# Kernel optimization log

Hardware: AMD Instinct MI355X
Metric: run time of the kernel (lower is better)

Reference implementation:

```python
import jax, jax.numpy as jnp
import numpy as np
from jax.scipy.special import gammaln, digamma


def setup_inputs() -> dict:
    key = jax.random.key(0)
    k1, k2 = jax.random.split(key)
    N, M, D = 512, 512, 256
    # Dirichlet concentration parameters: strictly positive
    v_alpha = jax.random.uniform(k1, (N, D), dtype=jnp.float32)
    t_alpha = jax.random.uniform(k2, (M, D), dtype=jnp.float32)
    return {"v_alpha": v_alpha, "t_alpha": t_alpha}


def _compute_kl(v_alpha, t_alpha):
    # v_alpha, t_alpha broadcast to (..., D); returns (...,) KL(Dir(v)||Dir(t))
    eps = 1e-08
    v = v_alpha + eps
    t = t_alpha + eps
    sum_v = v.sum(axis=-1)
    sum_t = t.sum(axis=-1)
    first = (gammaln(t).sum(axis=-1) + gammaln(sum_v)
             - gammaln(sum_t) - gammaln(v).sum(axis=-1))
    second = ((v - t) * (digamma(v) - digamma(sum_v)[..., None])).sum(axis=-1)
    return first + second


def reference(v_alpha, t_alpha):
    # Pairwise JS divergence between all (t_row, v_row) pairs.
    # Original: v.repeat(M,1) / t.repeat_interleave(N) then view(M, N)
    # -> equivalent to broadcasting t over axis 0, v over axis 1.
    v = v_alpha[None, :, :]   # (1, N, D)
    t = t_alpha[:, None, :]   # (M, 1, D)
    m = 0.5 * (v + t)         # (M, N, D)
    jsd = 0.5 * _compute_kl(v, m) + 0.5 * _compute_kl(t, m)  # (M, N)
    return 1.0 - jsd
```

## Files before the change

### kernel.cpp

```cpp
#include <hip/hip_runtime.h>

#define D 256
#define NV 512
#define NT 512
#define EPS 1e-8f
#define HALF_EPS 5e-9f
#define LN2 0.69314718055994531f

#define C0 0.28468287047291920f
#define C1 0.70315664064524320f
#define C2 0.24517887805011740f
#define C3 (-0.03936734194028790f)
#define C4 0.00932941036738560f
#define C5 (-0.00261463332905590f)
#define C6 0.00080356830356760f
#define C0E 0.28460998445f
#define C1E 0.69577526404f
#define C2E 0.24751123064f

#define LSTRIDE 68

__device__ __forceinline__ float rcpf(float x) { return __builtin_amdgcn_rcpf(x); }

__device__ __forceinline__ float stirling_lgamma(float y) {
    float r = rcpf(y), r2 = r * r;
    float ln = LN2 * __log2f(y);
    return (y - 0.5f) * ln - y + 0.91893853320467f
         + r * (0.08333333333f - 0.00277777778f * r2);
}

__device__ __forceinline__ float stirling_digamma(float y) {
    float r = rcpf(y), r2 = r * r;
    return LN2 * __log2f(y) - 0.5f * r - r2 * (0.08333333333f - 0.00833333333f * r2);
}

__global__ __launch_bounds__(256) void row_stats(
    const float* __restrict__ va, const float* __restrict__ ta,
    float* __restrict__ dgv, float* __restrict__ dgt,
    float* __restrict__ rv,  float* __restrict__ rt)
{
    int r = blockIdx.x;
    const float* row; float* dgrow; float* sc;
    if (r < NV) { row = va + r * D; dgrow = dgv + r * D; sc = rv + r * 4; }
    else { int q = r - NV; row = ta + q * D; dgrow = dgt + q * D; sc = rt + q * 4; }

    int d = threadIdx.x;
    float raw = row[d];
    float x = raw + EPS;

    float y = x + 4.0f;
    float ry = rcpf(y), ry2 = ry * ry;
    float psi = LN2 * __log2f(y) - 0.5f * ry - ry2 * (0.08333333333f - 0.00833333333f * ry2);
    psi -= rcpf(x) + rcpf(x + 1.0f) + rcpf(x + 2.0f) + rcpf(x + 3.0f);
    dgrow[d] = psi;

    float s = x - 0.5f;
    float q6 = fmaf(C6, s, C5);
    q6 = fmaf(q6, s, C4); q6 = fmaf(q6, s, C3); q6 = fmaf(q6, s, C2); q6 = fmaf(q6, s, C1);
    float g = fmaf(q6, s, C0) - LN2 * __log2f(x * (x + 1.0f));

    float S = raw, G = g, P = raw * psi, W = psi;
    #pragma unroll
    for (int off = 32; off > 0; off >>= 1) {
        S += __shfl_down(S, off, 64);
        G += __shfl_down(G, off, 64);
        P += __shfl_down(P, off, 64);
        W += __shfl_down(W, off, 64);
    }
    __shared__ float red[4][4];
    int wid = d >> 6, lane = d & 63;
    if (lane == 0) { red[0][wid] = S; red[1][wid] = G; red[2][wid] = P; red[3][wid] = W; }
    __syncthreads();
    if (d == 0) {
        float S4 = red[0][0] + red[0][1] + red[0][2] + red[0][3];
        float G4 = red[1][0] + red[1][1] + red[1][2] + red[1][3];
        float P4 = red[2][0] + red[2][1] + red[2][2] + red[2][3];
        float W4 = red[3][0] + red[3][1] + red[3][2] + red[3][3];
        float Se = S4 + 256.0f * EPS;
        float A = 0.5f * (stirling_lgamma(Se) - G4) + 0.25f * P4 + (0.25f * EPS) * W4;
        *(float4*)sc = make_float4(S4, A, stirling_digamma(Se), 0.0f);
    }
}

__global__ __launch_bounds__(256, 4) void jsd_pairs(
    const float* __restrict__ va, const float* __restrict__ ta,
    const float* __restrict__ dgv, const float* __restrict__ dgt,
    const float* __restrict__ rv,  const float* __restrict__ rt,
    float* __restrict__ out)
{
    __shared__ float vs[16 * LSTRIDE];
    __shared__ float gv[16 * LSTRIDE];
    __shared__ float ts[16 * LSTRIDE];
    __shared__ float gt[16 * LSTRIDE];

    const int tid = threadIdx.x;
    const int j0 = blockIdx.x * 16;
    const int i0 = blockIdx.y * 16;

    const int tj = tid & 15;
    const int ti = tid >> 4;

    const float* vp = vs + tj * LSTRIDE;
    const float* gp = gv + tj * LSTRIDE;
    const float* tp = ts + ti * LSTRIDE;
    const float* hp = gt + ti * LSTRIDE;
    const int ldst = ti * LSTRIDE + (tj << 2);

    float accM2a = 0.0f, accM2b = 0.0f;
    float accLa = 0.0f, accLb = 0.0f;
    float xsa = 0.0f, xsb = 0.0f;

    for (int h = 0; h < 4; ++h) {
        if (h) __syncthreads();
        {
            int goff = (h << 6) + (tj << 2);
            float4 a = *(const float4*)(va  + (j0 + ti) * D + goff);
            float4 b = *(const float4*)(dgv + (j0 + ti) * D + goff);
            float4 e = *(const float4*)(ta  + (i0 + ti) * D + goff);
            float4 f = *(const float4*)(dgt + (i0 + ti) * D + goff);
            a.x = fmaf(0.5f, a.x, HALF_EPS); a.y = fmaf(0.5f, a.y, HALF_EPS);
            a.z = fmaf(0.5f, a.z, HALF_EPS); a.w = fmaf(0.5f, a.w, HALF_EPS);
            e.x = fmaf(0.5f, e.x, HALF_EPS); e.y = fmaf(0.5f, e.y, HALF_EPS);
            e.z = fmaf(0.5f, e.z, HALF_EPS); e.w = fmaf(0.5f, e.w, HALF_EPS);
            *(float4*)(vs + ldst) = a;
            *(float4*)(gv + ldst) = b;
            *(float4*)(ts + ldst) = e;
            *(float4*)(gt + ldst) = f;
        }
        __syncthreads();

        #pragma unroll
        for (int c = 0; c < 16; ++c) {
            float4 v4 = *(const float4*)(vp + (c << 2));
            float4 g4 = *(const float4*)(gp + (c << 2));
            float4 t4 = *(const float4*)(tp + (c << 2));
            float4 h4 = *(const float4*)(hp + (c << 2));

            float m0 = v4.x + t4.x, m1 = v4.y + t4.y;
            float m2 = v4.z + t4.z, m3 = v4.w + t4.w;

            accM2a = fmaf(m0, m0, accM2a); accM2b = fmaf(m1, m1, accM2b);
            accM2a = fmaf(m2, m2, accM2a); accM2b = fmaf(m3, m3, accM2b);

            float w0 = fmaf(m0, m0, m0), w1 = fmaf(m1, m1, m1);
            float w2 = fmaf(m2, m2, m2), w3 = fmaf(m3, m3, m3);
            float lg = __log2f((w0 * w1) * (w2 * w3));
            if (c & 1) accLb += lg; else accLa += lg;

            xsa = fmaf(t4.x, g4.x, xsa); xsb = fmaf(t4.y, g4.y, xsb);
            xsa = fmaf(t4.z, g4.z, xsa); xsb = fmaf(t4.w, g4.w, xsb);
            xsa = fmaf(v4.x, h4.x, xsa); xsb = fmaf(v4.y, h4.y, xsb);
            xsa = fmaf(v4.z, h4.z, xsa); xsb = fmaf(v4.w, h4.w, xsb);
        }
    }

    const int j = j0 + tj, i = i0 + ti;
    float4 RJ = *(const float4*)(rv + j * 4);
    float4 RI = *(const float4*)(rt + i * 4);
    float Sv = RJ.x, Av = RJ.y, dgSv = RJ.z;
    float St = RI.x, At = RI.y, dgSt = RI.z;

    float M1 = fmaf(0.5f, Sv + St, 256.0f * EPS);
    float S1 = M1 - 128.0f;
    float S2 = (accM2a + accM2b) - M1 + 64.0f;
    float sumlg = fmaf(C1E, S1, 256.0f * C0E) + C2E * S2 - LN2 * (accLa + accLb);

    float jsd = sumlg - stirling_lgamma(M1) + Av + At
              - 0.5f * (xsa + xsb)
              + 0.25f * (Sv - St) * (dgSt - dgSv);

    out[i * 512 + j] = 1.0f - jsd;
}

extern "C" void kernel_launch(void* const* d_in, const int* in_sizes, int n_in,
                              void* d_out, int out_size, void* d_ws, size_t ws_size,
                              hipStream_t stream) {
    const float* va = (const float*)d_in[0];
    const float* ta = (const float*)d_in[1];
    float* ws  = (float*)d_ws;
    float* dgv = ws;
    float* dgt = ws + NV * D;
    float* rv  = ws + (NV + NT) * D;
    float* rt  = rv + NV * 4;
    float* out = (float*)d_out;

    row_stats<<<NV + NT, 256, 0, stream>>>(va, ta, dgv, dgt, rv, rt);
    jsd_pairs<<<dim3(32, 32), 256, 0, stream>>>(va, ta, dgv, dgt, rv, rt, out);
}
```

Measured before the change: 71.79 us.

## Offload bilinear cross terms to bf16 MFMA with split-precision hi/lo operands

Rewrites the pairwise bilinear terms (t·psi_v, v·psi_t and the m² quadratic) as a single matrix product, computed with bf16 MFMA instructions over concatenated hi/lo split operands laid out by row_stats. The quadratic term is split into per-row sums of squares plus a cross term folded into the product, so the scalar inner loop only keeps the log accumulation and no longer stages the digamma arrays in LDS. This cuts VALU work and LDS traffic in the pair kernel. In exchange it adds extra workspace writes in the stats kernel and some precision loss from the bf16 split.

```diff
diff --git a/kernel.cpp b/kernel.cpp
--- a/kernel.cpp
+++ b/kernel.cpp
@@ -3,6 +3,7 @@
 #define D 256
 #define NV 512
 #define NT 512
+#define KCAT 1536
 #define EPS 1e-8f
 #define HALF_EPS 5e-9f
 #define LN2 0.69314718055994531f
@@ -20,7 +21,19 @@
 
 #define LSTRIDE 68
 
+typedef float f32x4 __attribute__((ext_vector_type(4)));
+typedef short s16x8 __attribute__((ext_vector_type(8)));
+typedef unsigned short u16;
+
 __device__ __forceinline__ float rcpf(float x) { return __builtin_amdgcn_rcpf(x); }
+
+__device__ __forceinline__ u16 f2bf(float f) {
+    unsigned int u = __float_as_uint(f);
+    return (u16)((u + 0x7FFFu + ((u >> 16) & 1u)) >> 16);
+}
+__device__ __forceinline__ float bf2f(u16 b) {
+    return __uint_as_float(((unsigned int)b) << 16);
+}
 
 __device__ __forceinline__ float stirling_lgamma(float y) {
     float r = rcpf(y), r2 = r * r;
@@ -36,13 +49,15 @@
 
 __global__ __launch_bounds__(256) void row_stats(
     const float* __restrict__ va, const float* __restrict__ ta,
-    float* __restrict__ dgv, float* __restrict__ dgt,
-    float* __restrict__ rv,  float* __restrict__ rt)
+    u16* __restrict__ Acat, u16* __restrict__ Bcat,
+    float* __restrict__ rv, float* __restrict__ rt)
 {
     int r = blockIdx.x;
-    const float* row; float* dgrow; float* sc;
-    if (r < NV) { row = va + r * D; dgrow = dgv + r * D; sc = rv + r * 4; }
-    else { int q = r - NV; row = ta + q * D; dgrow = dgt + q * D; sc = rt + q * 4; }
+    bool isV = (r < NV);
+    int rr = isV ? r : r - NV;
+    const float* row = (isV ? va : ta) + rr * D;
+    float* sc = (isV ? rv : rt) + rr * 4;
+    u16* cat = (isV ? Bcat : Acat) + rr * KCAT;
 
     int d = threadIdx.x;
     float raw = row[d];
@@ -52,121 +67,131 @@
     float ry = rcpf(y), ry2 = ry * ry;
     float psi = LN2 * __log2f(y) - 0.5f * ry - ry2 * (0.08333333333f - 0.00833333333f * ry2);
     psi -= rcpf(x) + rcpf(x + 1.0f) + rcpf(x + 2.0f) + rcpf(x + 3.0f);
-    dgrow[d] = psi;
 
     float s = x - 0.5f;
     float q6 = fmaf(C6, s, C5);
     q6 = fmaf(q6, s, C4); q6 = fmaf(q6, s, C3); q6 = fmaf(q6, s, C2); q6 = fmaf(q6, s, C1);
     float g = fmaf(q6, s, C0) - LN2 * __log2f(x * (x + 1.0f));
 
-    float S = raw, G = g, P = raw * psi, W = psi;
+    float pm = psi - C2E * x;
+    u16 xh = f2bf(x);  u16 xl = f2bf(x - bf2f(xh));
+    u16 ph = f2bf(pm); u16 pl = f2bf(pm - bf2f(ph));
+    if (isV) {
+        cat[d] = ph; cat[d+256] = pl; cat[d+512] = ph;
+        cat[d+768] = xh; cat[d+1024] = xl; cat[d+1280] = xh;
+    } else {
+        cat[d] = xh; cat[d+256] = xh; cat[d+512] = xl;
+        cat[d+768] = ph; cat[d+1024] = ph; cat[d+1280] = pl;
+    }
+
+    float vh = fmaf(0.5f, raw, HALF_EPS);
+    float S = raw, G = g, P = x * psi, Q = vh * vh;
     #pragma unroll
     for (int off = 32; off > 0; off >>= 1) {
         S += __shfl_down(S, off, 64);
         G += __shfl_down(G, off, 64);
         P += __shfl_down(P, off, 64);
-        W += __shfl_down(W, off, 64);
+        Q += __shfl_down(Q, off, 64);
     }
     __shared__ float red[4][4];
     int wid = d >> 6, lane = d & 63;
-    if (lane == 0) { red[0][wid] = S; red[1][wid] = G; red[2][wid] = P; red[3][wid] = W; }
+    if (lane == 0) { red[0][wid] = S; red[1][wid] = G; red[2][wid] = P; red[3][wid] = Q; }
     __syncthreads();
     if (d == 0) {
         float S4 = red[0][0] + red[0][1] + red[0][2] + red[0][3];
         float G4 = red[1][0] + red[1][1] + red[1][2] + red[1][3];
         float P4 = red[2][0] + red[2][1] + red[2][2] + red[2][3];
-        float W4 = red[3][0] + red[3][1] + red[3][2] + red[3][3];
+        float Q4 = red[3][0] + red[3][1] + red[3][2] + red[3][3];
         float Se = S4 + 256.0f * EPS;
-        float A = 0.5f * (stirling_lgamma(Se) - G4) + 0.25f * P4 + (0.25f * EPS) * W4;
-        *(float4*)sc = make_float4(S4, A, stirling_digamma(Se), 0.0f);
+        float A = 0.5f * (stirling_lgamma(Se) - G4) + 0.25f * P4;
+        *(float4*)sc = make_float4(S4, A, stirling_digamma(Se), Q4);
     }
 }
 
 __global__ __launch_bounds__(256, 4) void jsd_pairs(
     const float* __restrict__ va, const float* __restrict__ ta,
-    const float* __restrict__ dgv, const float* __restrict__ dgt,
-    const float* __restrict__ rv,  const float* __restrict__ rt,
+    const u16* __restrict__ Acat, const u16* __restrict__ Bcat,
+    const float* __restrict__ rv, const float* __restrict__ rt,
     float* __restrict__ out)
 {
     __shared__ float vs[16 * LSTRIDE];
-    __shared__ float gv[16 * LSTRIDE];
     __shared__ float ts[16 * LSTRIDE];
-    __shared__ float gt[16 * LSTRIDE];
+    __shared__ float red[4 * 256];
 
     const int tid = threadIdx.x;
     const int j0 = blockIdx.x * 16;
     const int i0 = blockIdx.y * 16;
+    const int w = tid >> 6, l = tid & 63;
+
+    {
+        f32x4 acc = {0.0f, 0.0f, 0.0f, 0.0f};
+        const u16* Ap = Acat + (i0 + (l & 15)) * KCAT + w * 384 + ((l >> 4) << 3);
+        const u16* Bp = Bcat + (j0 + (l & 15)) * KCAT + w * 384 + ((l >> 4) << 3);
+        #pragma unroll
+        for (int st = 0; st < 12; ++st) {
+            s16x8 a = *(const s16x8*)(Ap + (st << 5));
+            s16x8 b = *(const s16x8*)(Bp + (st << 5));
+            acc = __builtin_amdgcn_mfma_f32_16x16x32_bf16(a, b, acc, 0, 0, 0);
+        }
+        int base = w * 256 + ((l >> 4) << 6) + (l & 15);
+        red[base]      = acc[0];
+        red[base + 16] = acc[1];
+        red[base + 32] = acc[2];
+        red[base + 48] = acc[3];
+    }
 
     const int tj = tid & 15;
     const int ti = tid >> 4;
-
     const float* vp = vs + tj * LSTRIDE;
-    const float* gp = gv + tj * LSTRIDE;
     const float* tp = ts + ti * LSTRIDE;
-    const float* hp = gt + ti * LSTRIDE;
     const int ldst = ti * LSTRIDE + (tj << 2);
 
-    float accM2a = 0.0f, accM2b = 0.0f;
     float accLa = 0.0f, accLb = 0.0f;
-    float xsa = 0.0f, xsb = 0.0f;
 
     for (int h = 0; h < 4; ++h) {
         if (h) __syncthreads();
         {
             int goff = (h << 6) + (tj << 2);
-            float4 a = *(const float4*)(va  + (j0 + ti) * D + goff);
-            float4 b = *(const float4*)(dgv + (j0 + ti) * D + goff);
-            float4 e = *(const float4*)(ta  + (i0 + ti) * D + goff);
-            float4 f = *(const float4*)(dgt + (i0 + ti) * D + goff);
+            float4 a = *(const float4*)(va + (j0 + ti) * D + goff);
+            float4 e = *(const float4*)(ta + (i0 + ti) * D + goff);
             a.x = fmaf(0.5f, a.x, HALF_EPS); a.y = fmaf(0.5f, a.y, HALF_EPS);
             a.z = fmaf(0.5f, a.z, HALF_EPS); a.w = fmaf(0.5f, a.w, HALF_EPS);
             e.x = fmaf(0.5f, e.x, HALF_EPS); e.y = fmaf(0.5f, e.y, HALF_EPS);
             e.z = fmaf(0.5f, e.z, HALF_EPS); e.w = fmaf(0.5f, e.w, HALF_EPS);
             *(float4*)(vs + ldst) = a;
-            *(float4*)(gv + ldst) = b;
             *(float4*)(ts + ldst) = e;
-            *(float4*)(gt + ldst) = f;
         }
         __syncthreads();
 
         #pragma unroll
         for (int c = 0; c < 16; ++c) {
             float4 v4 = *(const float4*)(vp + (c << 2));
-            float4 g4 = *(const float4*)(gp + (c << 2));
             float4 t4 = *(const float4*)(tp + (c << 2));
-            float4 h4 = *(const float4*)(hp + (c << 2));
-
             float m0 = v4.x + t4.x, m1 = v4.y + t4.y;
             float m2 = v4.z + t4.z, m3 = v4.w + t4.w;
-
-            accM2a = fmaf(m0, m0, accM2a); accM2b = fmaf(m1, m1, accM2b);
-            accM2a = fmaf(m2, m2, accM2a); accM2b = fmaf(m3, m3, accM2b);
-
             float w0 = fmaf(m0, m0, m0), w1 = fmaf(m1, m1, m1);
             float w2 = fmaf(m2, m2, m2), w3 = fmaf(m3, m3, m3);
             float lg = __log2f((w0 * w1) * (w2 * w3));
             if (c & 1) accLb += lg; else accLa += lg;
-
-            xsa = fmaf(t4.x, g4.x, xsa); xsb = fmaf(t4.y, g4.y, xsb);
-            xsa = fmaf(t4.z, g4.z, xsa); xsb = fmaf(t4.w, g4.w, xsb);
-            xsa = fmaf(v4.x, h4.x, xsa); xsb = fmaf(v4.y, h4.y, xsb);
-            xsa = fmaf(v4.z, h4.z, xsa); xsb = fmaf(v4.w, h4.w, xsb);
         }
     }
+
+    const int idx = ti * 16 + tj;
+    float W = red[idx] + red[256 + idx] + red[512 + idx] + red[768 + idx];
 
     const int j = j0 + tj, i = i0 + ti;
     float4 RJ = *(const float4*)(rv + j * 4);
     float4 RI = *(const float4*)(rt + i * 4);
-    float Sv = RJ.x, Av = RJ.y, dgSv = RJ.z;
-    float St = RI.x, At = RI.y, dgSt = RI.z;
+    float Sv = RJ.x, Av = RJ.y, dgSv = RJ.z, Qv = RJ.w;
+    float St = RI.x, At = RI.y, dgSt = RI.z, Qt = RI.w;
 
     float M1 = fmaf(0.5f, Sv + St, 256.0f * EPS);
     float S1 = M1 - 128.0f;
-    float S2 = (accM2a + accM2b) - M1 + 64.0f;
-    float sumlg = fmaf(C1E, S1, 256.0f * C0E) + C2E * S2 - LN2 * (accLa + accLb);
+    float quad = Qv + Qt - M1 + 64.0f;
+    float sumlg = fmaf(C1E, S1, 256.0f * C0E) + C2E * quad - LN2 * (accLa + accLb);
 
     float jsd = sumlg - stirling_lgamma(M1) + Av + At
-              - 0.5f * (xsa + xsb)
+              - 0.25f * W
               + 0.25f * (Sv - St) * (dgSt - dgSv);
 
     out[i * 512 + j] = 1.0f - jsd;
@@ -178,12 +203,12 @@
     const float* va = (const float*)d_in[0];
     const float* ta = (const float*)d_in[1];
     float* ws  = (float*)d_ws;
-    float* dgv = ws;
-    float* dgt = ws + NV * D;
-    float* rv  = ws + (NV + NT) * D;
-    float* rt  = rv + NV * 4;
+    float* rv  = ws;
+    float* rt  = ws + NV * 4;
+    u16*   Acat = (u16*)((char*)d_ws + 16384);
+    u16*   Bcat = (u16*)((char*)d_ws + 16384 + NV * KCAT * 2);
     float* out = (float*)d_out;
 
-    row_stats<<<NV + NT, 256, 0, stream>>>(va, ta, dgv, dgt, rv, rt);
-    jsd_pairs<<<dim3(32, 32), 256, 0, stream>>>(va, ta, dgv, dgt, rv, rt, out);
-}
+    row_stats<<<NV + NT, 256, 0, stream>>>(va, ta, Acat, Bcat, rv, rt);
+    jsd_pairs<<<dim3(32, 32), 256, 0, stream>>>(va, ta, Acat, Bcat, rv, rt, out);
+}
```

After: 76.44 us. +6.5%, slower.
